# Kernel tuning notes

Measured on AMD Instinct MI355X. Metric: run time of the kernel, lower is better.

Reference implementation:

```python
import jax, jax.numpy as jnp
import numpy as np

B, T, K = 1024, 512, 64  # batch, max_seq_len, num_tags


def setup_inputs() -> dict:
    key = jax.random.key(0)
    k1, k2, k3, k4 = jax.random.split(key, 4)
    logits = jax.random.normal(k1, (B, T, K), dtype=jnp.float32)
    trans = jax.random.normal(k2, (K, K), dtype=jnp.float32) * 0.1  # self._crf_weights
    gold = jax.random.randint(k3, (B, T), 0, K)
    # training sentences contain at least 2 words (per the assignment comment)
    seq_len = jax.random.randint(k4, (B,), 2, T + 1)
    return {"logits": logits, "trans": trans, "gold": gold, "seq_len": seq_len}


def reference(logits, trans, gold, seq_len):
    # crf_loss: loss = -crf_log_likelihood(...) / batch_size
    Bsz, Tlen, _ = logits.shape
    pos = jnp.arange(Tlen)
    valid = pos[None, :] < seq_len[:, None]  # [B, T]

    # first_loss: sum of unary scores at gold tags over valid positions
    unary = jnp.take_along_axis(logits, gold[..., None], axis=2)[..., 0]  # [B, T]
    first = jnp.sum(jnp.where(valid, unary, 0.0))

    # second_loss: sum of transition scores trans[gold_t, gold_{t+1}] for t+1 < seq_len
    pair = trans[gold[:, :-1], gold[:, 1:]]  # [B, T-1]
    valid_pair = pos[None, :-1] < (seq_len - 1)[:, None]
    second = jnp.sum(jnp.where(valid_pair, pair, 0.0))

    # third_loss: log-partition via forward recurrence
    # alpha_new[a] = logsumexp_b(trans[a, b] + alpha[b]) + logits[:, t, a]
    # (note: source reduces over axis=1 of (trans + alpha), i.e. the second index)
    def step(alpha, xs):
        t, lt = xs  # lt: [B, K] logits at time t
        new = jax.nn.logsumexp(trans[None, :, :] + alpha[:, None, :], axis=2) + lt
        alpha = jnp.where((t < seq_len)[:, None], new, alpha)
        return alpha, None

    alpha0 = logits[:, 0, :]                         # [B, K]
    ts = jnp.arange(1, Tlen)
    rest = jnp.swapaxes(logits[:, 1:, :], 0, 1)      # [T-1, B, K]
    alpha_final, _ = jax.lax.scan(step, alpha0, (ts, rest))
    third = jnp.sum(jax.nn.logsumexp(alpha_final, axis=1))

    log_like = first + second - third
    return -log_like / Bsz
```

## Files before the change

### kernel.cpp

```cpp
#include <hip/hip_runtime.h>

#define BB 1024
#define TT 512
#define KK 64
#define CH 8

typedef _Float16 f16x8 __attribute__((ext_vector_type(8)));
typedef float f32x4 __attribute__((ext_vector_type(4)));

__device__ __forceinline__ float wave_sum(float v) {
#pragma unroll
    for (int off = 1; off < 64; off <<= 1) v += __shfl_xor(v, off);
    return v;
}

__device__ __forceinline__ float wave_max(float v) {
#pragma unroll
    for (int off = 1; off < 64; off <<= 1) v = fmaxf(v, __shfl_xor(v, off));
    return v;
}

#define MFMA16(A, B, C) __builtin_amdgcn_mfma_f32_16x16x32_f16((A), (B), (C), 0, 0, 0)

__global__ void __launch_bounds__(64)
__attribute__((amdgpu_waves_per_eu(1, 1)))
crf_fwd(
    const float* __restrict__ logits,
    const float* __restrict__ trans,
    const int* __restrict__ gold,
    const int* __restrict__ seq_len,
    float* __restrict__ ws)
{
    __shared__ __align__(16) _Float16 plds[KK];
    const int b = blockIdx.x;
    const int j = threadIdx.x & 63;
    const float* lg = logits + (size_t)b * (TT * KK);
    const int* gd = gold + (size_t)b * TT;
    const int L = seq_len[b];

    const int i = j & 15;
    const int g = j >> 4;
    const bool sel1 = (i & 1) != 0;
    const bool sel2 = (i & 2) != 0;
    const bool sel4 = (i & 4) != 0;
    const bool sel8 = (i & 8) != 0;

    float af = 0.0f, asec = 0.0f;
#pragma unroll
    for (int c = 0; c < TT / 64; ++c) {
        int t = c * 64 + j;
        if (t < L) {
            int g0 = gd[t];
            af += lg[t * KK + g0];
            if (t + 1 < L) {
                int g1 = gd[t + 1];
                asec += trans[g0 * KK + g1];
            }
        }
    }

    const int baserow = ((i >> 2) << 4) + (i & 3);
    f16x8 A00, A01, A10, A11, A20, A21, A30, A31;
#define LDA(rr, cc, DST) { \
    const float* rp_ = trans + (size_t)(baserow + 4 * (rr)) * KK + 32 * (cc) + 8 * g; \
    f32x4 u0 = *(const f32x4*)rp_; f32x4 u1 = *(const f32x4*)(rp_ + 4); \
    DST[0] = (_Float16)__expf(u0.x); DST[1] = (_Float16)__expf(u0.y); \
    DST[2] = (_Float16)__expf(u0.z); DST[3] = (_Float16)__expf(u0.w); \
    DST[4] = (_Float16)__expf(u1.x); DST[5] = (_Float16)__expf(u1.y); \
    DST[6] = (_Float16)__expf(u1.z); DST[7] = (_Float16)__expf(u1.w); }
    LDA(0, 0, A00) LDA(0, 1, A01)
    LDA(1, 0, A10) LDA(1, 1, A11)
    LDA(2, 0, A20) LDA(2, 1, A21)
    LDA(3, 0, A30) LDA(3, 1, A31)
#undef LDA

    float a0 = lg[j];
    float mx = wave_max(a0);
    float p0 = __expf(a0 - mx);
    plds[j] = (_Float16)p0;
    int Etot = 0;

    f32x4 nl0, nl1;
    nl0.x = lg[1 * KK + j]; nl0.y = lg[2 * KK + j];
    nl0.z = lg[3 * KK + j]; nl0.w = lg[4 * KK + j];
    nl1.x = lg[5 * KK + j]; nl1.y = lg[6 * KK + j];
    nl1.z = lg[7 * KK + j]; nl1.w = lg[8 * KK + j];

#define STEP(EL) { \
    const f16x8* pb_ = (const f16x8*)plds; \
    f16x8 B0 = pb_[g]; \
    f16x8 B1 = pb_[g + 4]; \
    f32x4 D0 = {0.f, 0.f, 0.f, 0.f}, D1 = {0.f, 0.f, 0.f, 0.f}; \
    f32x4 D2 = {0.f, 0.f, 0.f, 0.f}, D3 = {0.f, 0.f, 0.f, 0.f}; \
    D0 = MFMA16(A00, B0, D0); D1 = MFMA16(A10, B0, D1); \
    D2 = MFMA16(A20, B0, D2); D3 = MFMA16(A30, B0, D3); \
    D0 = MFMA16(A01, B1, D0); D1 = MFMA16(A11, B1, D1); \
    D2 = MFMA16(A21, B1, D2); D3 = MFMA16(A31, B1, D3); \
    float t0_ = sel1 ? D0[1] : D0[0]; float t1_ = sel1 ? D0[3] : D0[2]; \
    float s0_ = sel2 ? t1_ : t0_; \
    float t2_ = sel1 ? D1[1] : D1[0]; float t3_ = sel1 ? D1[3] : D1[2]; \
    float s1_ = sel2 ? t3_ : t2_; \
    float t4_ = sel1 ? D2[1] : D2[0]; float t5_ = sel1 ? D2[3] : D2[2]; \
    float s2_ = sel2 ? t5_ : t4_; \
    float t6_ = sel1 ? D3[1] : D3[0]; float t7_ = sel1 ? D3[3] : D3[2]; \
    float s3_ = sel2 ? t7_ : t6_; \
    float sa_ = sel4 ? s1_ : s0_; float sb_ = sel4 ? s3_ : s2_; \
    float s_ = sel8 ? sb_ : sa_; \
    float pn = s_ * (EL); \
    unsigned sb = (unsigned)__builtin_amdgcn_readfirstlane((int)__float_as_uint(pn)); \
    int ee = (int)((sb >> 23) & 255u) - 127; \
    Etot += ee; \
    float scl = __uint_as_float((unsigned)((127 - ee) << 23)); \
    plds[j] = (_Float16)(pn * scl); }

    int t0 = 1;
    for (; t0 + CH <= L; t0 += CH) {
        asm volatile("" : "+v"(A00), "+v"(A01), "+v"(A10), "+v"(A11),
                          "+v"(A20), "+v"(A21), "+v"(A30), "+v"(A31));

        f32x4 el0, el1;
        el0.x = __expf(nl0.x); el0.y = __expf(nl0.y);
        el0.z = __expf(nl0.z); el0.w = __expf(nl0.w);
        el1.x = __expf(nl1.x); el1.y = __expf(nl1.y);
        el1.z = __expf(nl1.z); el1.w = __expf(nl1.w);

        {
            int tn = t0 + CH;
            int c0 = tn + 0; c0 = (c0 > TT - 1) ? TT - 1 : c0;
            int c1 = tn + 1; c1 = (c1 > TT - 1) ? TT - 1 : c1;
            int c2 = tn + 2; c2 = (c2 > TT - 1) ? TT - 1 : c2;
            int c3 = tn + 3; c3 = (c3 > TT - 1) ? TT - 1 : c3;
            int c4 = tn + 4; c4 = (c4 > TT - 1) ? TT - 1 : c4;
            int c5 = tn + 5; c5 = (c5 > TT - 1) ? TT - 1 : c5;
            int c6 = tn + 6; c6 = (c6 > TT - 1) ? TT - 1 : c6;
            int c7 = tn + 7; c7 = (c7 > TT - 1) ? TT - 1 : c7;
            nl0.x = lg[c0 * KK + j]; nl0.y = lg[c1 * KK + j];
            nl0.z = lg[c2 * KK + j]; nl0.w = lg[c3 * KK + j];
            nl1.x = lg[c4 * KK + j]; nl1.y = lg[c5 * KK + j];
            nl1.z = lg[c6 * KK + j]; nl1.w = lg[c7 * KK + j];
        }

        STEP(el0.x) STEP(el0.y) STEP(el0.z) STEP(el0.w)
        STEP(el1.x) STEP(el1.y) STEP(el1.z) STEP(el1.w)
    }

    if (t0 < L) {
        f32x4 el0, el1;
        el0.x = __expf(nl0.x); el0.y = __expf(nl0.y);
        el0.z = __expf(nl0.z); el0.w = __expf(nl0.w);
        el1.x = __expf(nl1.x); el1.y = __expf(nl1.y);
        el1.z = __expf(nl1.z); el1.w = __expf(nl1.w);
        if (t0 + 0 < L) { STEP(el0.x) }
        if (t0 + 1 < L) { STEP(el0.y) }
        if (t0 + 2 < L) { STEP(el0.z) }
        if (t0 + 3 < L) { STEP(el0.w) }
        if (t0 + 4 < L) { STEP(el1.x) }
        if (t0 + 5 < L) { STEP(el1.y) }
        if (t0 + 6 < L) { STEP(el1.z) }
    }
#undef STEP

    float pfin = (float)plds[j];
    float sump = wave_sum(pfin);
    float third_b = mx + (float)Etot * 0.6931471805599453f + __logf(sump);
    float first_b = wave_sum(af);
    float second_b = wave_sum(asec);

    if (j == 0) {
        ws[b] = (third_b - first_b - second_b) * (1.0f / (float)BB);
    }
}

__global__ void crf_reduce(const float* __restrict__ ws, float* __restrict__ out) {
    int tid = threadIdx.x;
    float v = ws[tid] + ws[tid + 256] + ws[tid + 512] + ws[tid + 768];
    v = wave_sum(v);
    __shared__ float sm[4];
    if ((tid & 63) == 0) sm[tid >> 6] = v;
    __syncthreads();
    if (tid == 0) out[0] = (sm[0] + sm[1]) + (sm[2] + sm[3]);
}

extern "C" void kernel_launch(void* const* d_in, const int* in_sizes, int n_in,
                              void* d_out, int out_size, void* d_ws, size_t ws_size,
                              hipStream_t stream) {
    const float* logits = (const float*)d_in[0];
    const float* trans  = (const float*)d_in[1];
    const int*   gold   = (const int*)d_in[2];
    const int*   slen   = (const int*)d_in[3];
    float* out = (float*)d_out;
    float* ws = (float*)d_ws;

    hipLaunchKernelGGL(crf_fwd, dim3(BB), dim3(64), 0, stream,
                       logits, trans, gold, slen, ws);
    hipLaunchKernelGGL(crf_reduce, dim3(1), dim3(256), 0, stream, ws, out);
}
```

Before: 106.8 us.

## Replace single-wave MFMA recurrence with 4-wave fp32 FMA matvec and barriers

Each batch row now runs on a 256-thread block instead of one wave. Every thread computes a 16-element fp32 dot product of exp(trans) with the probability vector, combines partials across 4 lanes with DPP, and writes to a double-buffered LDS vector. The fp16 MFMA matvec and the lane-select tree go away, and renormalisation now reads element 0 of the previous vector. This raises precision and spreads the work over more lanes, but it adds a workgroup barrier on every time step, which may dominate the latency of the serial recurrence.

```diff
diff --git a/kernel.cpp b/kernel.cpp
--- a/kernel.cpp
+++ b/kernel.cpp
@@ -5,7 +5,6 @@
 #define KK 64
 #define CH 8
 
-typedef _Float16 f16x8 __attribute__((ext_vector_type(8)));
 typedef float f32x4 __attribute__((ext_vector_type(4)));
 
 __device__ __forceinline__ float wave_sum(float v) {
@@ -20,10 +19,21 @@
     return v;
 }
 
-#define MFMA16(A, B, C) __builtin_amdgcn_mfma_f32_16x16x32_f16((A), (B), (C), 0, 0, 0)
-
-__global__ void __launch_bounds__(64)
-__attribute__((amdgpu_waves_per_eu(1, 1)))
+#if __has_builtin(__builtin_amdgcn_mov_dpp)
+__device__ __forceinline__ float dpp_xor1_f(float x) {
+    return __uint_as_float((unsigned)__builtin_amdgcn_mov_dpp(
+        (int)__float_as_uint(x), 0xB1, 0xF, 0xF, true));
+}
+__device__ __forceinline__ float dpp_xor2_f(float x) {
+    return __uint_as_float((unsigned)__builtin_amdgcn_mov_dpp(
+        (int)__float_as_uint(x), 0x4E, 0xF, 0xF, true));
+}
+#else
+__device__ __forceinline__ float dpp_xor1_f(float x) { return __shfl_xor(x, 1); }
+__device__ __forceinline__ float dpp_xor2_f(float x) { return __shfl_xor(x, 2); }
+#endif
+
+__global__ void __launch_bounds__(256)
 crf_fwd(
     const float* __restrict__ logits,
     const float* __restrict__ trans,
@@ -31,24 +41,24 @@
     const int* __restrict__ seq_len,
     float* __restrict__ ws)
 {
-    __shared__ __align__(16) _Float16 plds[KK];
+    __shared__ __align__(16) float buf[2][KK];
+    __shared__ float mxs;
+    __shared__ float redA[4], redB[4];
+
     const int b = blockIdx.x;
-    const int j = threadIdx.x & 63;
+    const int tid = threadIdx.x;
+    const int u = tid & 63;
+    const int w = tid >> 6;
+    const int myrow = (w << 4) | (u >> 2);
+    const int c = u & 3;
     const float* lg = logits + (size_t)b * (TT * KK);
     const int* gd = gold + (size_t)b * TT;
     const int L = seq_len[b];
 
-    const int i = j & 15;
-    const int g = j >> 4;
-    const bool sel1 = (i & 1) != 0;
-    const bool sel2 = (i & 2) != 0;
-    const bool sel4 = (i & 4) != 0;
-    const bool sel8 = (i & 8) != 0;
-
     float af = 0.0f, asec = 0.0f;
 #pragma unroll
-    for (int c = 0; c < TT / 64; ++c) {
-        int t = c * 64 + j;
+    for (int q = 0; q < TT / 256; ++q) {
+        int t = q * 256 + tid;
         if (t < L) {
             int g0 = gd[t];
             af += lg[t * KK + g0];
@@ -59,65 +69,71 @@
         }
     }
 
-    const int baserow = ((i >> 2) << 4) + (i & 3);
-    f16x8 A00, A01, A10, A11, A20, A21, A30, A31;
-#define LDA(rr, cc, DST) { \
-    const float* rp_ = trans + (size_t)(baserow + 4 * (rr)) * KK + 32 * (cc) + 8 * g; \
-    f32x4 u0 = *(const f32x4*)rp_; f32x4 u1 = *(const f32x4*)(rp_ + 4); \
-    DST[0] = (_Float16)__expf(u0.x); DST[1] = (_Float16)__expf(u0.y); \
-    DST[2] = (_Float16)__expf(u0.z); DST[3] = (_Float16)__expf(u0.w); \
-    DST[4] = (_Float16)__expf(u1.x); DST[5] = (_Float16)__expf(u1.y); \
-    DST[6] = (_Float16)__expf(u1.z); DST[7] = (_Float16)__expf(u1.w); }
-    LDA(0, 0, A00) LDA(0, 1, A01)
-    LDA(1, 0, A10) LDA(1, 1, A11)
-    LDA(2, 0, A20) LDA(2, 1, A21)
-    LDA(3, 0, A30) LDA(3, 1, A31)
-#undef LDA
-
-    float a0 = lg[j];
-    float mx = wave_max(a0);
-    float p0 = __expf(a0 - mx);
-    plds[j] = (_Float16)p0;
+    f32x4 Ea, Eb, Ec, Ed;
+    {
+        const float* rp = trans + (size_t)myrow * KK + (c << 4);
+        f32x4 v0 = *(const f32x4*)(rp + 0);
+        f32x4 v1 = *(const f32x4*)(rp + 4);
+        f32x4 v2 = *(const f32x4*)(rp + 8);
+        f32x4 v3 = *(const f32x4*)(rp + 12);
+        Ea.x = __expf(v0.x); Ea.y = __expf(v0.y); Ea.z = __expf(v0.z); Ea.w = __expf(v0.w);
+        Eb.x = __expf(v1.x); Eb.y = __expf(v1.y); Eb.z = __expf(v1.z); Eb.w = __expf(v1.w);
+        Ec.x = __expf(v2.x); Ec.y = __expf(v2.y); Ec.z = __expf(v2.z); Ec.w = __expf(v2.w);
+        Ed.x = __expf(v3.x); Ed.y = __expf(v3.y); Ed.z = __expf(v3.z); Ed.w = __expf(v3.w);
+    }
+
+    if (w == 0) {
+        float a0 = lg[u];
+        float mx = wave_max(a0);
+        buf[0][u] = __expf(a0 - mx);
+        if (u == 0) mxs = mx;
+    }
+
+    f32x4 nl0, nl1;
+    nl0.x = lg[1 * KK + myrow]; nl0.y = lg[2 * KK + myrow];
+    nl0.z = lg[3 * KK + myrow]; nl0.w = lg[4 * KK + myrow];
+    nl1.x = lg[5 * KK + myrow]; nl1.y = lg[6 * KK + myrow];
+    nl1.z = lg[7 * KK + myrow]; nl1.w = lg[8 * KK + myrow];
+
     int Etot = 0;
-
-    f32x4 nl0, nl1;
-    nl0.x = lg[1 * KK + j]; nl0.y = lg[2 * KK + j];
-    nl0.z = lg[3 * KK + j]; nl0.w = lg[4 * KK + j];
-    nl1.x = lg[5 * KK + j]; nl1.y = lg[6 * KK + j];
-    nl1.z = lg[7 * KK + j]; nl1.w = lg[8 * KK + j];
+    int par = 0;
+
+    asm volatile("s_waitcnt lgkmcnt(0)" ::: "memory");
+    __builtin_amdgcn_s_barrier();
+    asm volatile("" ::: "memory");
 
 #define STEP(EL) { \
-    const f16x8* pb_ = (const f16x8*)plds; \
-    f16x8 B0 = pb_[g]; \
-    f16x8 B1 = pb_[g + 4]; \
-    f32x4 D0 = {0.f, 0.f, 0.f, 0.f}, D1 = {0.f, 0.f, 0.f, 0.f}; \
-    f32x4 D2 = {0.f, 0.f, 0.f, 0.f}, D3 = {0.f, 0.f, 0.f, 0.f}; \
-    D0 = MFMA16(A00, B0, D0); D1 = MFMA16(A10, B0, D1); \
-    D2 = MFMA16(A20, B0, D2); D3 = MFMA16(A30, B0, D3); \
-    D0 = MFMA16(A01, B1, D0); D1 = MFMA16(A11, B1, D1); \
-    D2 = MFMA16(A21, B1, D2); D3 = MFMA16(A31, B1, D3); \
-    float t0_ = sel1 ? D0[1] : D0[0]; float t1_ = sel1 ? D0[3] : D0[2]; \
-    float s0_ = sel2 ? t1_ : t0_; \
-    float t2_ = sel1 ? D1[1] : D1[0]; float t3_ = sel1 ? D1[3] : D1[2]; \
-    float s1_ = sel2 ? t3_ : t2_; \
-    float t4_ = sel1 ? D2[1] : D2[0]; float t5_ = sel1 ? D2[3] : D2[2]; \
-    float s2_ = sel2 ? t5_ : t4_; \
-    float t6_ = sel1 ? D3[1] : D3[0]; float t7_ = sel1 ? D3[3] : D3[2]; \
-    float s3_ = sel2 ? t7_ : t6_; \
-    float sa_ = sel4 ? s1_ : s0_; float sb_ = sel4 ? s3_ : s2_; \
-    float s_ = sel8 ? sb_ : sa_; \
-    float pn = s_ * (EL); \
-    unsigned sb = (unsigned)__builtin_amdgcn_readfirstlane((int)__float_as_uint(pn)); \
-    int ee = (int)((sb >> 23) & 255u) - 127; \
-    Etot += ee; \
-    float scl = __uint_as_float((unsigned)((127 - ee) << 23)); \
-    plds[j] = (_Float16)(pn * scl); }
+    const float* br_ = &buf[par][0]; \
+    float* bw_ = &buf[par ^ 1][0]; \
+     \
+    float p0_ = br_[0]; \
+    unsigned pb_ = __float_as_uint(p0_); \
+    int ee_ = (int)((pb_ >> 23) & 255u) - 127; \
+    float scl_ = __uint_as_float((unsigned)((127 - ee_) << 23)); \
+    Etot += ee_; \
+     \
+    const f32x4* bs_ = (const f32x4*)(br_ + (c << 4)); \
+    f32x4 P0_ = bs_[0], P1_ = bs_[1], P2_ = bs_[2], P3_ = bs_[3]; \
+    float A0_ = Ea.x * P0_.x, A1_ = Eb.x * P1_.x; \
+    float A2_ = Ec.x * P2_.x, A3_ = Ed.x * P3_.x; \
+    A0_ = fmaf(Ea.y, P0_.y, A0_); A1_ = fmaf(Eb.y, P1_.y, A1_); \
+    A2_ = fmaf(Ec.y, P2_.y, A2_); A3_ = fmaf(Ed.y, P3_.y, A3_); \
+    A0_ = fmaf(Ea.z, P0_.z, A0_); A1_ = fmaf(Eb.z, P1_.z, A1_); \
+    A2_ = fmaf(Ec.z, P2_.z, A2_); A3_ = fmaf(Ed.z, P3_.z, A3_); \
+    A0_ = fmaf(Ea.w, P0_.w, A0_); A1_ = fmaf(Eb.w, P1_.w, A1_); \
+    A2_ = fmaf(Ec.w, P2_.w, A2_); A3_ = fmaf(Ed.w, P3_.w, A3_); \
+    float s4_ = (A0_ + A1_) + (A2_ + A3_); \
+    float sq_ = s4_ + dpp_xor1_f(s4_); \
+    sq_ = sq_ + dpp_xor2_f(sq_);             \
+    float pn_ = sq_ * (EL) * scl_; \
+    bw_[myrow] = pn_;    \
+    asm volatile("s_waitcnt lgkmcnt(0)" ::: "memory"); \
+    __builtin_amdgcn_s_barrier(); \
+    asm volatile("" ::: "memory"); \
+    par ^= 1; }
 
     int t0 = 1;
     for (; t0 + CH <= L; t0 += CH) {
-        asm volatile("" : "+v"(A00), "+v"(A01), "+v"(A10), "+v"(A11),
-                          "+v"(A20), "+v"(A21), "+v"(A30), "+v"(A31));
-
         f32x4 el0, el1;
         el0.x = __expf(nl0.x); el0.y = __expf(nl0.y);
         el0.z = __expf(nl0.z); el0.w = __expf(nl0.w);
@@ -134,10 +150,10 @@
             int c5 = tn + 5; c5 = (c5 > TT - 1) ? TT - 1 : c5;
             int c6 = tn + 6; c6 = (c6 > TT - 1) ? TT - 1 : c6;
             int c7 = tn + 7; c7 = (c7 > TT - 1) ? TT - 1 : c7;
-            nl0.x = lg[c0 * KK + j]; nl0.y = lg[c1 * KK + j];
-            nl0.z = lg[c2 * KK + j]; nl0.w = lg[c3 * KK + j];
-            nl1.x = lg[c4 * KK + j]; nl1.y = lg[c5 * KK + j];
-            nl1.z = lg[c6 * KK + j]; nl1.w = lg[c7 * KK + j];
+            nl0.x = lg[c0 * KK + myrow]; nl0.y = lg[c1 * KK + myrow];
+            nl0.z = lg[c2 * KK + myrow]; nl0.w = lg[c3 * KK + myrow];
+            nl1.x = lg[c4 * KK + myrow]; nl1.y = lg[c5 * KK + myrow];
+            nl1.z = lg[c6 * KK + myrow]; nl1.w = lg[c7 * KK + myrow];
         }
 
         STEP(el0.x) STEP(el0.y) STEP(el0.z) STEP(el0.w)
@@ -160,14 +176,20 @@
     }
 #undef STEP
 
-    float pfin = (float)plds[j];
-    float sump = wave_sum(pfin);
-    float third_b = mx + (float)Etot * 0.6931471805599453f + __logf(sump);
-    float first_b = wave_sum(af);
-    float second_b = wave_sum(asec);
-
-    if (j == 0) {
-        ws[b] = (third_b - first_b - second_b) * (1.0f / (float)BB);
+    float afs = wave_sum(af);
+    float ass = wave_sum(asec);
+    if (u == 0) { redA[w] = afs; redB[w] = ass; }
+    __syncthreads();
+
+    if (w == 0) {
+        float pf = buf[par][u];
+        float sum = wave_sum(pf);
+        if (u == 0) {
+            float third = mxs + (float)Etot * 0.6931471805599453f + __logf(sum);
+            float first = (redA[0] + redA[1]) + (redA[2] + redA[3]);
+            float second = (redB[0] + redB[1]) + (redB[2] + redB[3]);
+            ws[b] = (third - first - second) * (1.0f / (float)BB);
+        }
     }
 }
 
@@ -191,7 +213,7 @@
     float* out = (float*)d_out;
     float* ws = (float*)d_ws;
 
-    hipLaunchKernelGGL(crf_fwd, dim3(BB), dim3(64), 0, stream,
+    hipLaunchKernelGGL(crf_fwd, dim3(BB), dim3(256), 0, stream,
                        logits, trans, gold, slen, ws);
     hipLaunchKernelGGL(crf_reduce, dim3(1), dim3(256), 0, stream, ws, out);
 }
```

Result: slower. 131.6 us (+23.3%).

## Replace fp16 MFMA recurrence with fp32 packed-FMA matvec and DPP reduction

Applied to the files above, without the earlier changes.

Each step's 64x64 exp-space matvec no longer uses fp16 MFMA instructions followed by a select tree. Instead, each lane holds a 4-row by 16-column slice of exp(trans) in fp32 and accumulates with packed fp32 FMAs, then combines partial sums across lanes with DPP xor shuffles. Renormalisation now happens once per 8-step chunk, folded into the first step's emission scale, instead of a readfirstlane at every step. This aims to shorten the serial per-step latency chain and gain fp32 accuracy, at the cost of many more VALU FMAs and registers per step, plus a wider LDS vector read.

```diff
diff --git a/kernel.cpp b/kernel.cpp
--- a/kernel.cpp
+++ b/kernel.cpp
@@ -5,8 +5,11 @@
 #define KK 64
 #define CH 8
 
-typedef _Float16 f16x8 __attribute__((ext_vector_type(8)));
 typedef float f32x4 __attribute__((ext_vector_type(4)));
+typedef float f32x2 __attribute__((ext_vector_type(2)));
+
+#define LO2(v4) __builtin_shufflevector((v4), (v4), 0, 1)
+#define HI2(v4) __builtin_shufflevector((v4), (v4), 2, 3)
 
 __device__ __forceinline__ float wave_sum(float v) {
 #pragma unroll
@@ -20,7 +23,19 @@
     return v;
 }
 
-#define MFMA16(A, B, C) __builtin_amdgcn_mfma_f32_16x16x32_f16((A), (B), (C), 0, 0, 0)
+#if __has_builtin(__builtin_amdgcn_mov_dpp)
+__device__ __forceinline__ float dpp_xor1_f(float x) {
+    return __uint_as_float((unsigned)__builtin_amdgcn_mov_dpp(
+        (int)__float_as_uint(x), 0xB1, 0xF, 0xF, true));
+}
+__device__ __forceinline__ float dpp_xor2_f(float x) {
+    return __uint_as_float((unsigned)__builtin_amdgcn_mov_dpp(
+        (int)__float_as_uint(x), 0x4E, 0xF, 0xF, true));
+}
+#else
+__device__ __forceinline__ float dpp_xor1_f(float x) { return __shfl_xor(x, 1); }
+__device__ __forceinline__ float dpp_xor2_f(float x) { return __shfl_xor(x, 2); }
+#endif
 
 __global__ void __launch_bounds__(64)
 __attribute__((amdgpu_waves_per_eu(1, 1)))
@@ -31,24 +46,20 @@
     const int* __restrict__ seq_len,
     float* __restrict__ ws)
 {
-    __shared__ __align__(16) _Float16 plds[KK];
+    __shared__ __align__(16) float buf[KK];
     const int b = blockIdx.x;
     const int j = threadIdx.x & 63;
+    const int qr = (j >> 2) << 2;
+    const int c = j & 3;
+    const int sc = c << 4;
     const float* lg = logits + (size_t)b * (TT * KK);
     const int* gd = gold + (size_t)b * TT;
     const int L = seq_len[b];
 
-    const int i = j & 15;
-    const int g = j >> 4;
-    const bool sel1 = (i & 1) != 0;
-    const bool sel2 = (i & 2) != 0;
-    const bool sel4 = (i & 4) != 0;
-    const bool sel8 = (i & 8) != 0;
-
     float af = 0.0f, asec = 0.0f;
 #pragma unroll
-    for (int c = 0; c < TT / 64; ++c) {
-        int t = c * 64 + j;
+    for (int q = 0; q < TT / 64; ++q) {
+        int t = q * 64 + j;
         if (t < L) {
             int g0 = gd[t];
             af += lg[t * KK + g0];
@@ -59,25 +70,27 @@
         }
     }
 
-    const int baserow = ((i >> 2) << 4) + (i & 3);
-    f16x8 A00, A01, A10, A11, A20, A21, A30, A31;
-#define LDA(rr, cc, DST) { \
-    const float* rp_ = trans + (size_t)(baserow + 4 * (rr)) * KK + 32 * (cc) + 8 * g; \
-    f32x4 u0 = *(const f32x4*)rp_; f32x4 u1 = *(const f32x4*)(rp_ + 4); \
-    DST[0] = (_Float16)__expf(u0.x); DST[1] = (_Float16)__expf(u0.y); \
-    DST[2] = (_Float16)__expf(u0.z); DST[3] = (_Float16)__expf(u0.w); \
-    DST[4] = (_Float16)__expf(u1.x); DST[5] = (_Float16)__expf(u1.y); \
-    DST[6] = (_Float16)__expf(u1.z); DST[7] = (_Float16)__expf(u1.w); }
-    LDA(0, 0, A00) LDA(0, 1, A01)
-    LDA(1, 0, A10) LDA(1, 1, A11)
-    LDA(2, 0, A20) LDA(2, 1, A21)
-    LDA(3, 0, A30) LDA(3, 1, A31)
-#undef LDA
+    f32x2 E00, E01, E02, E03, E04, E05, E06, E07;
+    f32x2 E10, E11, E12, E13, E14, E15, E16, E17;
+    f32x2 E20, E21, E22, E23, E24, E25, E26, E27;
+    f32x2 E30, E31, E32, E33, E34, E35, E36, E37;
+#define LDROW(RR, N0, N1, N2, N3, N4, N5, N6, N7) { \
+    const float* rp_ = trans + (size_t)(qr + (c ^ (RR))) * KK + sc; \
+    f32x4 v0 = *(const f32x4*)(rp_ + 0);  f32x4 v1 = *(const f32x4*)(rp_ + 4); \
+    f32x4 v2 = *(const f32x4*)(rp_ + 8);  f32x4 v3 = *(const f32x4*)(rp_ + 12); \
+    N0.x = __expf(v0.x); N0.y = __expf(v0.y); N1.x = __expf(v0.z); N1.y = __expf(v0.w); \
+    N2.x = __expf(v1.x); N2.y = __expf(v1.y); N3.x = __expf(v1.z); N3.y = __expf(v1.w); \
+    N4.x = __expf(v2.x); N4.y = __expf(v2.y); N5.x = __expf(v2.z); N5.y = __expf(v2.w); \
+    N6.x = __expf(v3.x); N6.y = __expf(v3.y); N7.x = __expf(v3.z); N7.y = __expf(v3.w); }
+    LDROW(0, E00, E01, E02, E03, E04, E05, E06, E07)
+    LDROW(1, E10, E11, E12, E13, E14, E15, E16, E17)
+    LDROW(2, E20, E21, E22, E23, E24, E25, E26, E27)
+    LDROW(3, E30, E31, E32, E33, E34, E35, E36, E37)
+#undef LDROW
 
     float a0 = lg[j];
     float mx = wave_max(a0);
-    float p0 = __expf(a0 - mx);
-    plds[j] = (_Float16)p0;
+    buf[j] = __expf(a0 - mx);
     int Etot = 0;
 
     f32x4 nl0, nl1;
@@ -86,37 +99,38 @@
     nl1.x = lg[5 * KK + j]; nl1.y = lg[6 * KK + j];
     nl1.z = lg[7 * KK + j]; nl1.w = lg[8 * KK + j];
 
+#define PK(EH, W, A) A = __builtin_elementwise_fma(EH, (W), A);
+
 #define STEP(EL) { \
-    const f16x8* pb_ = (const f16x8*)plds; \
-    f16x8 B0 = pb_[g]; \
-    f16x8 B1 = pb_[g + 4]; \
-    f32x4 D0 = {0.f, 0.f, 0.f, 0.f}, D1 = {0.f, 0.f, 0.f, 0.f}; \
-    f32x4 D2 = {0.f, 0.f, 0.f, 0.f}, D3 = {0.f, 0.f, 0.f, 0.f}; \
-    D0 = MFMA16(A00, B0, D0); D1 = MFMA16(A10, B0, D1); \
-    D2 = MFMA16(A20, B0, D2); D3 = MFMA16(A30, B0, D3); \
-    D0 = MFMA16(A01, B1, D0); D1 = MFMA16(A11, B1, D1); \
-    D2 = MFMA16(A21, B1, D2); D3 = MFMA16(A31, B1, D3); \
-    float t0_ = sel1 ? D0[1] : D0[0]; float t1_ = sel1 ? D0[3] : D0[2]; \
-    float s0_ = sel2 ? t1_ : t0_; \
-    float t2_ = sel1 ? D1[1] : D1[0]; float t3_ = sel1 ? D1[3] : D1[2]; \
-    float s1_ = sel2 ? t3_ : t2_; \
-    float t4_ = sel1 ? D2[1] : D2[0]; float t5_ = sel1 ? D2[3] : D2[2]; \
-    float s2_ = sel2 ? t5_ : t4_; \
-    float t6_ = sel1 ? D3[1] : D3[0]; float t7_ = sel1 ? D3[3] : D3[2]; \
-    float s3_ = sel2 ? t7_ : t6_; \
-    float sa_ = sel4 ? s1_ : s0_; float sb_ = sel4 ? s3_ : s2_; \
-    float s_ = sel8 ? sb_ : sa_; \
-    float pn = s_ * (EL); \
-    unsigned sb = (unsigned)__builtin_amdgcn_readfirstlane((int)__float_as_uint(pn)); \
-    int ee = (int)((sb >> 23) & 255u) - 127; \
-    Etot += ee; \
-    float scl = __uint_as_float((unsigned)((127 - ee) << 23)); \
-    plds[j] = (_Float16)(pn * scl); }
+    const f32x4* bs_ = (const f32x4*)(buf + sc); \
+    f32x4 W0_ = bs_[0], W1_ = bs_[1], W2_ = bs_[2], W3_ = bs_[3]; \
+    f32x2 a0_ = {0.f, 0.f}, a1_ = {0.f, 0.f}, a2_ = {0.f, 0.f}, a3_ = {0.f, 0.f}; \
+    PK(E00, LO2(W0_), a0_) PK(E10, LO2(W0_), a1_) PK(E20, LO2(W0_), a2_) PK(E30, LO2(W0_), a3_) \
+    PK(E01, HI2(W0_), a0_) PK(E11, HI2(W0_), a1_) PK(E21, HI2(W0_), a2_) PK(E31, HI2(W0_), a3_) \
+    PK(E02, LO2(W1_), a0_) PK(E12, LO2(W1_), a1_) PK(E22, LO2(W1_), a2_) PK(E32, LO2(W1_), a3_) \
+    PK(E03, HI2(W1_), a0_) PK(E13, HI2(W1_), a1_) PK(E23, HI2(W1_), a2_) PK(E33, HI2(W1_), a3_) \
+    PK(E04, LO2(W2_), a0_) PK(E14, LO2(W2_), a1_) PK(E24, LO2(W2_), a2_) PK(E34, LO2(W2_), a3_) \
+    PK(E05, HI2(W2_), a0_) PK(E15, HI2(W2_), a1_) PK(E25, HI2(W2_), a2_) PK(E35, HI2(W2_), a3_) \
+    PK(E06, LO2(W3_), a0_) PK(E16, LO2(W3_), a1_) PK(E26, LO2(W3_), a2_) PK(E36, LO2(W3_), a3_) \
+    PK(E07, HI2(W3_), a0_) PK(E17, HI2(W3_), a1_) PK(E27, HI2(W3_), a2_) PK(E37, HI2(W3_), a3_) \
+    float P0_ = a0_.x + a0_.y; float P1_ = a1_.x + a1_.y; \
+    float P2_ = a2_.x + a2_.y; float P3_ = a3_.x + a3_.y; \
+    float Q0_ = P0_ + dpp_xor1_f(P1_); \
+    float Q1_ = P2_ + dpp_xor1_f(P3_); \
+    float s_ = Q0_ + dpp_xor2_f(Q1_);        \
+    float pn_ = s_ * (EL); \
+    buf[j] = pn_; }
 
     int t0 = 1;
     for (; t0 + CH <= L; t0 += CH) {
-        asm volatile("" : "+v"(A00), "+v"(A01), "+v"(A10), "+v"(A11),
-                          "+v"(A20), "+v"(A21), "+v"(A30), "+v"(A31));
+        asm volatile("" : "+v"(E00), "+v"(E01), "+v"(E02), "+v"(E03),
+                          "+v"(E04), "+v"(E05), "+v"(E06), "+v"(E07),
+                          "+v"(E10), "+v"(E11), "+v"(E12), "+v"(E13),
+                          "+v"(E14), "+v"(E15), "+v"(E16), "+v"(E17));
+        asm volatile("" : "+v"(E20), "+v"(E21), "+v"(E22), "+v"(E23),
+                          "+v"(E24), "+v"(E25), "+v"(E26), "+v"(E27),
+                          "+v"(E30), "+v"(E31), "+v"(E32), "+v"(E33),
+                          "+v"(E34), "+v"(E35), "+v"(E36), "+v"(E37));
 
         f32x4 el0, el1;
         el0.x = __expf(nl0.x); el0.y = __expf(nl0.y);
@@ -140,6 +154,15 @@
             nl1.z = lg[c6 * KK + j]; nl1.w = lg[c7 * KK + j];
         }
 
+        {
+            float p00 = buf[0];
+            unsigned pb = __float_as_uint(p00);
+            int ee = (int)((pb >> 23) & 255u) - 127;
+            Etot += ee;
+            float scl = __uint_as_float((unsigned)((127 - ee) << 23));
+            el0.x *= scl;
+        }
+
         STEP(el0.x) STEP(el0.y) STEP(el0.z) STEP(el0.w)
         STEP(el1.x) STEP(el1.y) STEP(el1.z) STEP(el1.w)
     }
@@ -150,6 +173,14 @@
         el0.z = __expf(nl0.z); el0.w = __expf(nl0.w);
         el1.x = __expf(nl1.x); el1.y = __expf(nl1.y);
         el1.z = __expf(nl1.z); el1.w = __expf(nl1.w);
+        {
+            float p00 = buf[0];
+            unsigned pb = __float_as_uint(p00);
+            int ee = (int)((pb >> 23) & 255u) - 127;
+            Etot += ee;
+            float scl = __uint_as_float((unsigned)((127 - ee) << 23));
+            el0.x *= scl;
+        }
         if (t0 + 0 < L) { STEP(el0.x) }
         if (t0 + 1 < L) { STEP(el0.y) }
         if (t0 + 2 < L) { STEP(el0.z) }
@@ -159,8 +190,9 @@
         if (t0 + 6 < L) { STEP(el1.z) }
     }
 #undef STEP
-
-    float pfin = (float)plds[j];
+#undef PK
+
+    float pfin = buf[j];
     float sump = wave_sum(pfin);
     float third_b = mx + (float)Etot * 0.6931471805599453f + __logf(sump);
     float first_b = wave_sum(af);
```

Measured after the change: 86.37 us. 19.1% less time.
